# Performance work log

Measured on AMD Instinct MI355X. Metric: run time of the kernel, lower is better.

Reference implementation:

```python
import jax, jax.numpy as jnp
import numpy as np

FS = 512.0
T = 2048
CYC_PHA, CYC_AMP = 3, 6
NBINS = 18
PHA_BANDS = [(2.0 + 2.0 * k, 4.0 + 2.0 * k) for k in range(10)]
AMP_BANDS = [(30.0 + 12.0 * k, 42.0 + 12.0 * k) for k in range(10)]


def _design_filter(fs, low, high, cycle):
    # windowed-sinc bandpass, taps = cycle * fs / low (tensorpac cycle rule), forced odd
    n = int(cycle * fs / low)
    if n % 2 == 0:
        n += 1
    t = np.arange(n) - (n - 1) / 2.0
    lp = lambda fc: 2.0 * fc / fs * np.sinc(2.0 * fc / fs * t)
    h = (lp(high) - lp(low)) * np.hamming(n)
    fc = 0.5 * (low + high)
    h = h / np.abs(np.sum(h * np.exp(-2j * np.pi * fc / fs * t)))  # unit gain at band center
    return h.astype(np.float32)


def _build_kernels():
    filts = [_design_filter(FS, l, h, CYC_PHA) for l, h in PHA_BANDS] + \
            [_design_filter(FS, l, h, CYC_AMP) for l, h in AMP_BANDS]
    L = max(f.shape[0] for f in filts)
    padded = []
    for f in filts:
        p = L - f.shape[0]
        pl = p // 2
        padded.append(np.pad(f, (pl, p - pl)))
    return np.stack(padded)  # (F, L), L odd


def _conv_same(sig, kernels):
    # sig: (N, Tp), kernels: (F, L) -> (N, F, Tp); cross-correlation, 'same' padding (L odd)
    L = kernels.shape[1]
    pad = (L - 1) // 2
    return jax.lax.conv_general_dilated(
        sig[:, None, :], kernels[:, None, :], window_strides=(1,),
        padding=((pad, L - 1 - pad),), dimension_numbers=("NCH", "OIH", "NCH"))


def _analytic(x):
    # FFT-based Hilbert analytic signal along last axis
    n = x.shape[-1]
    h = np.zeros(n, np.float32)
    h[0] = 1.0
    if n % 2 == 0:
        h[n // 2] = 1.0
        h[1:n // 2] = 2.0
    else:
        h[1:(n + 1) // 2] = 2.0
    return jnp.fft.ifft(jnp.fft.fft(x, axis=-1) * h, axis=-1)


def _modulation_index(pha, amp):
    # Tort MI: pha (B,C,P,S,T), amp (B,C,A,S,T) -> (B,C,P,A)
    idx = jnp.clip(jnp.floor((pha + jnp.pi) / (2.0 * jnp.pi) * NBINS), 0, NBINS - 1).astype(jnp.int32)
    sums, cnts = [], []
    for b in range(NBINS):  # fixed small bin count
        m = (idx == b).astype(amp.dtype)                       # (B,C,P,S,T)
        sums.append(jnp.einsum('bcpst,bcast->bcpas', m, amp))  # (B,C,P,A,S)
        cnts.append(m.sum(-1))                                 # (B,C,P,S)
    amp_sum = jnp.stack(sums, -1)                              # (B,C,P,A,S,N)
    cnt = jnp.stack(cnts, -1)[:, :, :, None, :, :]             # (B,C,P,1,S,N)
    amp_mean = amp_sum / jnp.maximum(cnt, 1.0)
    p = amp_mean / jnp.maximum(amp_mean.sum(-1, keepdims=True), 1e-12)
    log_n = jnp.log(jnp.asarray(NBINS, amp.dtype))
    mi = (log_n + (p * jnp.log(jnp.maximum(p, 1e-12))).sum(-1)) / log_n
    return mi.mean(-1)  # average over segments


def setup_inputs() -> dict:
    key = jax.random.key(0)
    x = jax.random.normal(key, (4, 8, 4, T), dtype=jnp.float32)
    kernels = jnp.asarray(_build_kernels())
    return {"x": x, "kernels": kernels}


def reference(x, kernels):
    B, C, S, Tlen = x.shape
    npha = len(PHA_BANDS)
    pad = kernels.shape[1] - 1  # max_padlen (edge_mode)
    sig = x.reshape(B * C * S, Tlen)
    sig = jnp.pad(sig, ((0, 0), (pad, pad)), mode='reflect')
    # filtfilt_mode: average forward conv and time-reversed conv
    fwd = _conv_same(sig, kernels)
    bwd = _conv_same(sig[:, ::-1], kernels)[:, :, ::-1]
    filt = 0.5 * (fwd + bwd)
    filt = filt[:, :, pad:-pad]  # strip edge padding -> (N, F, T)
    ana = _analytic(filt)
    pha = jnp.arctan2(ana.imag[:, :npha], ana.real[:, :npha])
    amp = jnp.sqrt(ana.real[:, npha:] ** 2 + ana.imag[:, npha:] ** 2)
    pha = pha.reshape(B, C, npha, S, Tlen)
    amp = amp.reshape(B, C, len(AMP_BANDS), S, Tlen)
    return _modulation_index(pha, amp)
```

## Files before the change

### kernel.cpp

```cpp
#include <hip/hip_runtime.h>
#include <math.h>

#define TT 2048
#define LK 769
#define NF 20
#define NS 128
#define NB 18
#define NFFT 4096

typedef __attribute__((ext_vector_type(8))) short short8;
typedef __attribute__((ext_vector_type(4))) float f32x4;

__device__ __forceinline__ float2 cmul(float2 a, float2 b) {
  return make_float2(a.x * b.x - a.y * b.y, a.x * b.y + a.y * b.x);
}
__device__ __forceinline__ float2 cmulc(float2 a, float2 b) {
  return make_float2(a.x * b.x + a.y * b.y, a.y * b.x - a.x * b.y);
}
#define CADD(a, b) make_float2((a).x + (b).x, (a).y + (b).y)
#define CSUB(a, b) make_float2((a).x - (b).x, (a).y - (b).y)

__device__ __forceinline__ void fwd_r8(float2* z, const float2* __restrict__ tw,
                                       int tt, int Q) {
  const float C = 0.70710678118654752f;
  const int j = tt & (Q - 1);
  const int base = ((tt & ~(Q - 1)) << 3) + j;
  const float2 x0 = z[base],         x1 = z[base + Q];
  const float2 x2 = z[base + 2 * Q], x3 = z[base + 3 * Q];
  const float2 x4 = z[base + 4 * Q], x5 = z[base + 5 * Q];
  const float2 x6 = z[base + 6 * Q], x7 = z[base + 7 * Q];
  const float2 W1 = tw[4 * Q + j], W2 = tw[2 * Q + j], W4 = tw[Q + j];
  const float2 W3 = cmul(W1, W2);
  const float2 W5 = cmul(W1, W4);
  const float2 W6 = cmul(W2, W4);
  const float2 W7 = cmul(W3, W4);
  const float2 s0 = CADD(x0, x4), s1 = CSUB(x0, x4);
  const float2 s2 = CADD(x2, x6), s3 = CSUB(x2, x6);
  const float2 E0 = CADD(s0, s2), E2 = CSUB(s0, s2);
  const float2 E1 = make_float2(s1.x + s3.y, s1.y - s3.x);
  const float2 E3 = make_float2(s1.x - s3.y, s1.y + s3.x);
  const float2 t0 = CADD(x1, x5), t1 = CSUB(x1, x5);
  const float2 t2 = CADD(x3, x7), t3 = CSUB(x3, x7);
  const float2 O0 = CADD(t0, t2), O2 = CSUB(t0, t2);
  const float2 O1 = make_float2(t1.x + t3.y, t1.y - t3.x);
  const float2 O3 = make_float2(t1.x - t3.y, t1.y + t3.x);
  const float2 wO1 = make_float2(C * (O1.x + O1.y), C * (O1.y - O1.x));
  const float2 w3O3 = make_float2(C * (O3.y - O3.x), -C * (O3.x + O3.y));
  const float2 mO2 = make_float2(O2.y, -O2.x);
  const float2 y0 = CADD(E0, O0), y4 = CSUB(E0, O0);
  const float2 y1 = CADD(E1, wO1), y5 = CSUB(E1, wO1);
  const float2 y2 = CADD(E2, mO2), y6 = CSUB(E2, mO2);
  const float2 y3 = CADD(E3, w3O3), y7 = CSUB(E3, w3O3);
  z[base]         = y0;
  z[base + Q]     = cmul(y1, W1);
  z[base + 2 * Q] = cmul(y2, W2);
  z[base + 3 * Q] = cmul(y3, W3);
  z[base + 4 * Q] = cmul(y4, W4);
  z[base + 5 * Q] = cmul(y5, W5);
  z[base + 6 * Q] = cmul(y6, W6);
  z[base + 7 * Q] = cmul(y7, W7);
}

__device__ __forceinline__ void inv_r8(float2* z, const float2* __restrict__ tw,
                                       int tt, int Q) {
  const float C = 0.70710678118654752f;
  const int j = tt & (Q - 1);
  const int base = ((tt & ~(Q - 1)) << 3) + j;
  const float2 W1 = tw[4 * Q + j], W2 = tw[2 * Q + j], W4 = tw[Q + j];
  const float2 W3 = cmul(W1, W2);
  const float2 W5 = cmul(W1, W4);
  const float2 W6 = cmul(W2, W4);
  const float2 W7 = cmul(W3, W4);
  const float2 u0 = z[base];
  const float2 u1 = cmulc(z[base + Q], W1);
  const float2 u2 = cmulc(z[base + 2 * Q], W2);
  const float2 u3 = cmulc(z[base + 3 * Q], W3);
  const float2 u4 = cmulc(z[base + 4 * Q], W4);
  const float2 u5 = cmulc(z[base + 5 * Q], W5);
  const float2 u6 = cmulc(z[base + 6 * Q], W6);
  const float2 u7 = cmulc(z[base + 7 * Q], W7);
  const float2 s0 = CADD(u0, u4), s1 = CSUB(u0, u4);
  const float2 s2 = CADD(u2, u6), s3 = CSUB(u2, u6);
  const float2 E0 = CADD(s0, s2), E2 = CSUB(s0, s2);
  const float2 E1 = make_float2(s1.x - s3.y, s1.y + s3.x);
  const float2 E3 = make_float2(s1.x + s3.y, s1.y - s3.x);
  const float2 t0 = CADD(u1, u5), t1 = CSUB(u1, u5);
  const float2 t2 = CADD(u3, u7), t3 = CSUB(u3, u7);
  const float2 O0 = CADD(t0, t2), O2 = CSUB(t0, t2);
  const float2 O1 = make_float2(t1.x - t3.y, t1.y + t3.x);
  const float2 O3 = make_float2(t1.x + t3.y, t1.y - t3.x);
  const float2 nO1 = make_float2(C * (O1.x - O1.y), C * (O1.x + O1.y));
  const float2 n3O3 = make_float2(-C * (O3.x + O3.y), C * (O3.x - O3.y));
  const float2 iO2 = make_float2(-O2.y, O2.x);
  z[base]         = CADD(E0, O0);
  z[base + 4 * Q] = CSUB(E0, O0);
  z[base + Q]     = CADD(E1, nO1);
  z[base + 5 * Q] = CSUB(E1, nO1);
  z[base + 2 * Q] = CADD(E2, iO2);
  z[base + 6 * Q] = CSUB(E2, iO2);
  z[base + 3 * Q] = CADD(E3, n3O3);
  z[base + 7 * Q] = CSUB(E3, n3O3);
}

__global__ __launch_bounds__(256) void prep_kernel(float2* __restrict__ tw,
                                                   float* __restrict__ out) {
  const int i = blockIdx.x * 256 + threadIdx.x;
  if (i == 0) {
    tw[0] = make_float2(1.f, 0.f);
  } else {
    int half = 1 << (31 - __clz(i));
    int j = i - half;
    float ang = -3.14159265358979323846f * (float)j / (float)half;
    float s, c;
    sincosf(ang, &s, &c);
    tw[i] = make_float2(c, s);
  }
  if (i < 3200) out[i] = 0.f;
}

__global__ __launch_bounds__(256) void specf_kernel(const float* __restrict__ x,
                                                    const float* __restrict__ ker,
                                                    const float2* __restrict__ tw,
                                                    float2* __restrict__ Hc,
                                                    float2* __restrict__ Xs) {
  __shared__ __align__(16) float2 z[NFFT];
  const int tid = threadIdx.x;
  const int blk = blockIdx.x;
  if (blk < NF) {
    const float* kr = ker + blk * LK;
#pragma unroll
    for (int h = 0; h < 16; ++h) {
      int i = tid + 256 * h;
      float v = 0.f;
      if (i < LK) v = 0.5f * (kr[i] + kr[LK - 1 - i]);
      z[i] = make_float2(v, 0.f);
    }
  } else {
    const float* xr = x + (size_t)(blk - NF) * TT;
#pragma unroll
    for (int h = 0; h < 16; ++h) {
      int i = tid + 256 * h;
      float v = 0.f;
      if (i < 2816) {
        int m = i - 384;
        if (m < 0) m = -m;
        if (m > 2047) m = 4094 - m;
        v = xr[m];
      }
      z[i] = make_float2(v, 0.f);
    }
  }
  __syncthreads();
  fwd_r8(z, tw, tid, 512);
  fwd_r8(z, tw, tid + 256, 512);
  __syncthreads();
  fwd_r8(z, tw, tid, 64);
  fwd_r8(z, tw, tid + 256, 64);
  __builtin_amdgcn_wave_barrier();
  fwd_r8(z, tw, tid, 8);
  fwd_r8(z, tw, tid + 256, 8);
  __builtin_amdgcn_wave_barrier();
  fwd_r8(z, tw, tid, 1);
  fwd_r8(z, tw, tid + 256, 1);
  __syncthreads();
  if (blk < NF) {
    const float s = 1.0f / 4096.0f;
    float2* o = Hc + (size_t)blk * NFFT;
#pragma unroll
    for (int h = 0; h < 16; ++h) {
      int i = tid + 256 * h;
      float2 v = z[i];
      o[i] = make_float2(v.x * s, -v.y * s);
    }
  } else {
    float2* o = Xs + (size_t)(blk - NF) * NFFT;
#pragma unroll
    for (int h = 0; h < 16; ++h) {
      int i = tid + 256 * h;
      o[i] = z[i];
    }
  }
}

__global__ __launch_bounds__(256) void convhil_kernel(const float2* __restrict__ Xs,
                                                      const float2* __restrict__ Hc,
                                                      const float2* __restrict__ tw,
                                                      float* __restrict__ filt) {
  __shared__ __align__(16) float2 z[NFFT];
  const int tid = threadIdx.x;
  const int wv = tid >> 6;
  const int lane = tid & 63;
  const int ord = blockIdx.x;
  const int p = ord / NS;
  const int n = ord % NS;
  const int o1 = p;
  const int o2 = 10 + (9 - p);
  const float2* Xn = Xs + (size_t)n * NFFT;
  const float2* H1 = Hc + (size_t)o1 * NFFT;
  const float2* H2 = Hc + (size_t)o2 * NFFT;
#pragma unroll
  for (int h = 0; h < 16; ++h) {
    int i = tid + 256 * h;
    float2 Xv = Xn[i];
    float2 a = H1[i];
    float2 b = H2[i];
    float2 Cc = make_float2(a.x - b.y, a.y + b.x);
    z[i] = cmul(Xv, Cc);
  }
  __syncthreads();
  inv_r8(z, tw, tid, 1);
  inv_r8(z, tw, tid + 256, 1);
  __builtin_amdgcn_wave_barrier();
  inv_r8(z, tw, tid, 8);
  inv_r8(z, tw, tid + 256, 8);
  __builtin_amdgcn_wave_barrier();
  inv_r8(z, tw, tid, 64);
  inv_r8(z, tw, tid + 256, 64);
  __syncthreads();
  inv_r8(z, tw, tid, 512);
  inv_r8(z, tw, tid + 256, 512);
  __syncthreads();
  const int bA = 4 * tid;
  const int bB = 1024 + 4 * tid;
  float acc1A[4], acc1B[4], acc2A[4], acc2B[4];
#pragma unroll
  for (int r = 0; r < 4; ++r) {
    float2 vA = z[bA + r]; acc1A[r] = vA.x; acc2A[r] = vA.y;
    float2 vB = z[bB + r]; acc1B[r] = vB.x; acc2B[r] = vB.y;
  }
  __syncthreads();
  const float C = 0.70710678118654752f;
  fwd_r8(z, tw, tid, 256);
  __syncthreads();
  fwd_r8(z, tw, tid, 32);
  __builtin_amdgcn_wave_barrier();
  fwd_r8(z, tw, tid, 4);
  __builtin_amdgcn_wave_barrier();
#pragma unroll
  for (int h = 0; h < 2; ++h) {
    const int bf = 128 * wv + lane + 64 * h;
    const int base = bf << 2;
    const float2 x0 = z[base], x1 = z[base + 1];
    const float2 x2 = z[base + 2], x3 = z[base + 3];
    const float2 t0 = CADD(x0, x2), t1 = CSUB(x0, x2);
    const float2 t2 = CADD(x1, x3), t3 = CSUB(x1, x3);
    z[base]     = CADD(t0, t2);
    z[base + 1] = make_float2(t1.x + t3.y, t1.y - t3.x);
    z[base + 2] = CSUB(t0, t2);
    z[base + 3] = make_float2(t1.x - t3.y, t1.y + t3.x);
  }
  __builtin_amdgcn_wave_barrier();
#pragma unroll
  for (int i = 0; i < 8; ++i) {
    const int pp = 512 * wv + lane + 64 * i;
    if (pp != 0 && pp != 2) {
      if (pp & 2) { z[pp] = make_float2(0.f, 0.f); }
      else        { float2 v = z[pp]; z[pp] = make_float2(2.f * v.x, 2.f * v.y); }
    }
  }
  __builtin_amdgcn_wave_barrier();
#pragma unroll
  for (int h = 0; h < 2; ++h) {
    const int bf = 128 * wv + lane + 64 * h;
    const int base = bf << 2;
    const float2 u0 = z[base], u1 = z[base + 1];
    const float2 u2 = z[base + 2], u3 = z[base + 3];
    const float2 t0 = CADD(u0, u2), t1 = CSUB(u0, u2);
    const float2 t2 = CADD(u1, u3), t3 = CSUB(u1, u3);
    z[base]     = CADD(t0, t2);
    z[base + 1] = make_float2(t1.x - t3.y, t1.y + t3.x);
    z[base + 2] = CSUB(t0, t2);
    z[base + 3] = make_float2(t1.x + t3.y, t1.y - t3.x);
  }
  __builtin_amdgcn_wave_barrier();
  inv_r8(z, tw, tid, 4);
  __builtin_amdgcn_wave_barrier();
  inv_r8(z, tw, tid, 32);
  __builtin_amdgcn_wave_barrier();
  __syncthreads();
  inv_r8(z, tw, tid, 256);
  __syncthreads();
  (void)C;
  float* out1 = filt + ((size_t)n * NF + o1) * TT;
  float* out2 = filt + ((size_t)n * NF + o2) * TT;
  const float invN = 1.0f / 2048.0f;
  float phA[4], phB[4], amA[4], amB[4];
#pragma unroll
  for (int r = 0; r < 4; ++r) {
    float2 wvA = z[bA + r];
    float h1 = wvA.y * invN - acc2A[r];
    float h2 = acc1A[r] - wvA.x * invN;
    phA[r] = atan2f(h1, acc1A[r]);
    amA[r] = sqrtf(fmaf(acc2A[r], acc2A[r], h2 * h2));
    float2 wvB = z[bB + r];
    float g1 = wvB.y * invN - acc2B[r];
    float g2 = acc1B[r] - wvB.x * invN;
    phB[r] = atan2f(g1, acc1B[r]);
    amB[r] = sqrtf(fmaf(acc2B[r], acc2B[r], g2 * g2));
  }
  *(float4*)&out1[bA] = make_float4(phA[0], phA[1], phA[2], phA[3]);
  *(float4*)&out1[bB] = make_float4(phB[0], phB[1], phB[2], phB[3]);
  *(float4*)&out2[bA] = make_float4(amA[0], amA[1], amA[2], amA[3]);
  *(float4*)&out2[bB] = make_float4(amB[0], amB[1], amB[2], amB[3]);
}

__global__ __launch_bounds__(256) void mi_kernel(const float* __restrict__ filt,
                                                 float* __restrict__ out) {
  __shared__ __align__(16) unsigned int idx32[512];
  __shared__ float Cp[4][12][19];
  const int tid = threadIdx.x;
  const int wave = tid >> 6;
  const int lane = tid & 63;
  const int blk = blockIdx.x;
  const int bc = blk / 40, jp = blk % 40;
  const float* ph = filt + ((size_t)(bc * 4 + jp / 10) * NF + (jp % 10)) * TT;
  for (int g = tid; g < 512; g += 256) {
    float4 v = *(const float4*)&ph[4 * g];
    float vv[4] = {v.x, v.y, v.z, v.w};
    unsigned int packed = 0;
#pragma unroll
    for (int j = 0; j < 4; ++j) {
      int b = (int)floorf((vv[j] + 3.14159274f) / 6.2831855f * 18.0f);
      b = b < 0 ? 0 : (b > 17 ? 17 : b);
      packed |= ((unsigned int)b) << (8 * j);
    }
    idx32[g] = packed;
  }
  __syncthreads();
  const int n16 = lane & 15;
  const int quad = lane >> 4;
  const int aband = n16 < 10 ? n16 : 9;
  const int ja = (jp & 3) + 4 * aband;
  const float* aptr = filt + ((size_t)(bc * 4 + ja / 10) * NF + 10 + (ja % 10)) * TT
                      + quad * 8;
  const bool isAmp = (n16 < 10);
  const bool isOne = (n16 == 10);
  f32x4 acc0 = {0.f, 0.f, 0.f, 0.f};
  f32x4 acc1 = {0.f, 0.f, 0.f, 0.f};
  const int s0 = wave * 16, s1 = s0 + 16;
  float4 p0 = *(const float4*)(aptr + s0 * 32);
  float4 p1 = *(const float4*)(aptr + s0 * 32 + 4);
  for (int s = s0; s < s1; ++s) {
    float4 c0 = p0, c1 = p1;
    if (s < s1 - 1) {
      p0 = *(const float4*)(aptr + (s + 1) * 32);
      p1 = *(const float4*)(aptr + (s + 1) * 32 + 4);
    }
    float a[8] = {c0.x, c0.y, c0.z, c0.w, c1.x, c1.y, c1.z, c1.w};
    short8 ah, am_, al;
#pragma unroll
    for (int j = 0; j < 8; ++j) {
      float v = isAmp ? a[j] : (isOne ? 1.0f : 0.0f);
      unsigned int u = __float_as_uint(v);
      float h = __uint_as_float(u & 0xFFFF0000u);
      float r1 = v - h;
      unsigned int u2 = __float_as_uint(r1);
      float md = __uint_as_float(u2 & 0xFFFF0000u);
      float r2 = r1 - md;
      unsigned int u3 = __float_as_uint(r2);
      ah[j] = (short)(u >> 16);
      am_[j] = (short)(u2 >> 16);
      al[j] = (short)(u3 >> 16);
    }
    const int dw = s * 8 + quad * 2;
    unsigned int d0 = idx32[dw], d1 = idx32[dw + 1];
    short8 b0, b1;
#pragma unroll
    for (int j = 0; j < 8; ++j) {
      unsigned int byte = ((j < 4 ? d0 : d1) >> ((j & 3) * 8)) & 0xFFu;
      b0[j] = (byte == (unsigned int)n16) ? (short)0x3F80 : (short)0;
      b1[j] = (byte == (unsigned int)(n16 + 16)) ? (short)0x3F80 : (short)0;
    }
    acc0 = __builtin_amdgcn_mfma_f32_16x16x32_bf16(ah, b0, acc0, 0, 0, 0);
    acc0 = __builtin_amdgcn_mfma_f32_16x16x32_bf16(am_, b0, acc0, 0, 0, 0);
    acc0 = __builtin_amdgcn_mfma_f32_16x16x32_bf16(al, b0, acc0, 0, 0, 0);
    acc1 = __builtin_amdgcn_mfma_f32_16x16x32_bf16(ah, b1, acc1, 0, 0, 0);
    acc1 = __builtin_amdgcn_mfma_f32_16x16x32_bf16(am_, b1, acc1, 0, 0, 0);
    acc1 = __builtin_amdgcn_mfma_f32_16x16x32_bf16(al, b1, acc1, 0, 0, 0);
  }
#pragma unroll
  for (int r = 0; r < 4; ++r) {
    int row = quad * 4 + r;
    if (row < 11) {
      Cp[wave][row][n16] = acc0[r];
      if (n16 < 2) Cp[wave][row][16 + n16] = acc1[r];
    }
  }
  __syncthreads();
  if (tid < 10) {
    float tot = 0.f, mb_[18];
#pragma unroll
    for (int b = 0; b < 18; ++b) {
      float s = Cp[0][tid][b] + Cp[1][tid][b] + Cp[2][tid][b] + Cp[3][tid][b];
      float c = Cp[0][10][b] + Cp[1][10][b] + Cp[2][10][b] + Cp[3][10][b];
      float mb = s / fmaxf(c, 1.0f);
      mb_[b] = mb; tot += mb;
    }
    tot = fmaxf(tot, 1e-12f);
    float s = 0.f;
#pragma unroll
    for (int b = 0; b < 18; ++b) {
      float pb = mb_[b] / tot;
      s += pb * logf(fmaxf(pb, 1e-12f));
    }
    const float LOGN = 2.8903717578961645f;
    atomicAdd(&out[bc * 100 + (jp >> 2) * 10 + tid],
              0.25f * (LOGN + s) / LOGN);
  }
}

extern "C" void kernel_launch(void* const* d_in, const int* in_sizes, int n_in,
                              void* d_out, int out_size, void* d_ws, size_t ws_size,
                              hipStream_t stream) {
  (void)in_sizes; (void)n_in; (void)out_size; (void)ws_size;
  const float* x = (const float*)d_in[0];
  const float* ker = (const float*)d_in[1];
  float* out = (float*)d_out;
  float* filt = (float*)d_ws;
  float2* tw = (float2*)(filt + (size_t)NS * NF * TT);
  float2* Hc = tw + NFFT;
  float2* Xs = Hc + (size_t)NF * NFFT;

  prep_kernel<<<16, 256, 0, stream>>>(tw, out);
  specf_kernel<<<NF + NS, 256, 0, stream>>>(x, ker, tw, Hc, Xs);
  convhil_kernel<<<NS * 10, 256, 0, stream>>>(Xs, Hc, tw, filt);
  mi_kernel<<<32 * 40, 256, 0, stream>>>(filt, out);
}
```

Baseline: 125.9 us.

## Fuse phase binning into convhil, share amp loads across two phase bands

The Hilbert/conv kernel now quantizes phase into packed 8-bit bin indices and writes those, replacing the float phase stores, so the MI kernel reads 4x less phase data. The first inverse radix-8 stage is fused with the spectral multiply straight from global memory, and twiddle-free radix-8 variants replace the j=0 stages. The MI kernel handles two phase bands per block so each amplitude load and bf16 split is reused for twice the MFMA work, with half as many blocks and a swizzled block order. In exchange, per-thread register pressure in the MI kernel rises and there is a new workspace buffer.

```diff
diff --git a/kernel.cpp b/kernel.cpp
--- a/kernel.cpp
+++ b/kernel.cpp
@@ -61,6 +61,35 @@
   z[base + 7 * Q] = cmul(y7, W7);
 }
 
+__device__ __forceinline__ void fwd_r8_j0(float2* z, int base) {
+  const float C = 0.70710678118654752f;
+  const float2 x0 = z[base],     x1 = z[base + 1];
+  const float2 x2 = z[base + 2], x3 = z[base + 3];
+  const float2 x4 = z[base + 4], x5 = z[base + 5];
+  const float2 x6 = z[base + 6], x7 = z[base + 7];
+  const float2 s0 = CADD(x0, x4), s1 = CSUB(x0, x4);
+  const float2 s2 = CADD(x2, x6), s3 = CSUB(x2, x6);
+  const float2 E0 = CADD(s0, s2), E2 = CSUB(s0, s2);
+  const float2 E1 = make_float2(s1.x + s3.y, s1.y - s3.x);
+  const float2 E3 = make_float2(s1.x - s3.y, s1.y + s3.x);
+  const float2 t0 = CADD(x1, x5), t1 = CSUB(x1, x5);
+  const float2 t2 = CADD(x3, x7), t3 = CSUB(x3, x7);
+  const float2 O0 = CADD(t0, t2), O2 = CSUB(t0, t2);
+  const float2 O1 = make_float2(t1.x + t3.y, t1.y - t3.x);
+  const float2 O3 = make_float2(t1.x - t3.y, t1.y + t3.x);
+  const float2 wO1 = make_float2(C * (O1.x + O1.y), C * (O1.y - O1.x));
+  const float2 w3O3 = make_float2(C * (O3.y - O3.x), -C * (O3.x + O3.y));
+  const float2 mO2 = make_float2(O2.y, -O2.x);
+  z[base]     = CADD(E0, O0);
+  z[base + 4] = CSUB(E0, O0);
+  z[base + 1] = CADD(E1, wO1);
+  z[base + 5] = CSUB(E1, wO1);
+  z[base + 2] = CADD(E2, mO2);
+  z[base + 6] = CSUB(E2, mO2);
+  z[base + 3] = CADD(E3, w3O3);
+  z[base + 7] = CSUB(E3, w3O3);
+}
+
 __device__ __forceinline__ void inv_r8(float2* z, const float2* __restrict__ tw,
                                        int tt, int Q) {
   const float C = 0.70710678118654752f;
@@ -102,6 +131,47 @@
   z[base + 7 * Q] = CSUB(E3, n3O3);
 }
 
+__device__ __forceinline__ void inv8_j0_fused(float2* z,
+                                              const float2* __restrict__ Xn,
+                                              const float2* __restrict__ H1,
+                                              const float2* __restrict__ H2,
+                                              int b8) {
+  const float4* X4 = (const float4*)(Xn + b8);
+  const float4* A4 = (const float4*)(H1 + b8);
+  const float4* B4 = (const float4*)(H2 + b8);
+  float2 u[8];
+#pragma unroll
+  for (int q = 0; q < 4; ++q) {
+    float4 xv = X4[q], av = A4[q], bv = B4[q];
+    float2 Cc0 = make_float2(av.x - bv.y, av.y + bv.x);
+    float2 Cc1 = make_float2(av.z - bv.w, av.w + bv.z);
+    u[2 * q]     = cmul(make_float2(xv.x, xv.y), Cc0);
+    u[2 * q + 1] = cmul(make_float2(xv.z, xv.w), Cc1);
+  }
+  const float C = 0.70710678118654752f;
+  const float2 s0 = CADD(u[0], u[4]), s1 = CSUB(u[0], u[4]);
+  const float2 s2 = CADD(u[2], u[6]), s3 = CSUB(u[2], u[6]);
+  const float2 E0 = CADD(s0, s2), E2 = CSUB(s0, s2);
+  const float2 E1 = make_float2(s1.x - s3.y, s1.y + s3.x);
+  const float2 E3 = make_float2(s1.x + s3.y, s1.y - s3.x);
+  const float2 t0 = CADD(u[1], u[5]), t1 = CSUB(u[1], u[5]);
+  const float2 t2 = CADD(u[3], u[7]), t3 = CSUB(u[3], u[7]);
+  const float2 O0 = CADD(t0, t2), O2 = CSUB(t0, t2);
+  const float2 O1 = make_float2(t1.x - t3.y, t1.y + t3.x);
+  const float2 O3 = make_float2(t1.x + t3.y, t1.y - t3.x);
+  const float2 nO1 = make_float2(C * (O1.x - O1.y), C * (O1.x + O1.y));
+  const float2 n3O3 = make_float2(-C * (O3.x + O3.y), C * (O3.x - O3.y));
+  const float2 iO2 = make_float2(-O2.y, O2.x);
+  z[b8]     = CADD(E0, O0);
+  z[b8 + 4] = CSUB(E0, O0);
+  z[b8 + 1] = CADD(E1, nO1);
+  z[b8 + 5] = CSUB(E1, nO1);
+  z[b8 + 2] = CADD(E2, iO2);
+  z[b8 + 6] = CSUB(E2, iO2);
+  z[b8 + 3] = CADD(E3, n3O3);
+  z[b8 + 7] = CSUB(E3, n3O3);
+}
+
 __global__ __launch_bounds__(256) void prep_kernel(float2* __restrict__ tw,
                                                    float* __restrict__ out) {
   const int i = blockIdx.x * 256 + threadIdx.x;
@@ -160,8 +230,8 @@
   fwd_r8(z, tw, tid, 8);
   fwd_r8(z, tw, tid + 256, 8);
   __builtin_amdgcn_wave_barrier();
-  fwd_r8(z, tw, tid, 1);
-  fwd_r8(z, tw, tid + 256, 1);
+  fwd_r8_j0(z, tid << 3);
+  fwd_r8_j0(z, (tid + 256) << 3);
   __syncthreads();
   if (blk < NF) {
     const float s = 1.0f / 4096.0f;
@@ -185,7 +255,8 @@
 __global__ __launch_bounds__(256) void convhil_kernel(const float2* __restrict__ Xs,
                                                       const float2* __restrict__ Hc,
                                                       const float2* __restrict__ tw,
-                                                      float* __restrict__ filt) {
+                                                      float* __restrict__ filt,
+                                                      unsigned int* __restrict__ binp) {
   __shared__ __align__(16) float2 z[NFFT];
   const int tid = threadIdx.x;
   const int wv = tid >> 6;
@@ -198,18 +269,8 @@
   const float2* Xn = Xs + (size_t)n * NFFT;
   const float2* H1 = Hc + (size_t)o1 * NFFT;
   const float2* H2 = Hc + (size_t)o2 * NFFT;
-#pragma unroll
-  for (int h = 0; h < 16; ++h) {
-    int i = tid + 256 * h;
-    float2 Xv = Xn[i];
-    float2 a = H1[i];
-    float2 b = H2[i];
-    float2 Cc = make_float2(a.x - b.y, a.y + b.x);
-    z[i] = cmul(Xv, Cc);
-  }
-  __syncthreads();
-  inv_r8(z, tw, tid, 1);
-  inv_r8(z, tw, tid + 256, 1);
+  inv8_j0_fused(z, Xn, H1, H2, tid << 3);
+  inv8_j0_fused(z, Xn, H1, H2, (tid + 256) << 3);
   __builtin_amdgcn_wave_barrier();
   inv_r8(z, tw, tid, 8);
   inv_r8(z, tw, tid + 256, 8);
@@ -229,7 +290,6 @@
     float2 vB = z[bB + r]; acc1B[r] = vB.x; acc2B[r] = vB.y;
   }
   __syncthreads();
-  const float C = 0.70710678118654752f;
   fwd_r8(z, tw, tid, 256);
   __syncthreads();
   fwd_r8(z, tw, tid, 32);
@@ -280,69 +340,76 @@
   __syncthreads();
   inv_r8(z, tw, tid, 256);
   __syncthreads();
-  (void)C;
-  float* out1 = filt + ((size_t)n * NF + o1) * TT;
+  unsigned int* bp = binp + ((size_t)n * 10 + o1) * 512;
   float* out2 = filt + ((size_t)n * NF + o2) * TT;
   const float invN = 1.0f / 2048.0f;
-  float phA[4], phB[4], amA[4], amB[4];
+  float amA[4], amB[4];
+  unsigned int dA = 0, dB = 0;
 #pragma unroll
   for (int r = 0; r < 4; ++r) {
     float2 wvA = z[bA + r];
     float h1 = wvA.y * invN - acc2A[r];
     float h2 = acc1A[r] - wvA.x * invN;
-    phA[r] = atan2f(h1, acc1A[r]);
+    float phA = atan2f(h1, acc1A[r]);
     amA[r] = sqrtf(fmaf(acc2A[r], acc2A[r], h2 * h2));
+    int b = (int)floorf((phA + 3.14159274f) / 6.2831855f * 18.0f);
+    b = b < 0 ? 0 : (b > 17 ? 17 : b);
+    dA |= ((unsigned int)b) << (8 * r);
     float2 wvB = z[bB + r];
     float g1 = wvB.y * invN - acc2B[r];
     float g2 = acc1B[r] - wvB.x * invN;
-    phB[r] = atan2f(g1, acc1B[r]);
+    float phB = atan2f(g1, acc1B[r]);
     amB[r] = sqrtf(fmaf(acc2B[r], acc2B[r], g2 * g2));
-  }
-  *(float4*)&out1[bA] = make_float4(phA[0], phA[1], phA[2], phA[3]);
-  *(float4*)&out1[bB] = make_float4(phB[0], phB[1], phB[2], phB[3]);
+    int b2 = (int)floorf((phB + 3.14159274f) / 6.2831855f * 18.0f);
+    b2 = b2 < 0 ? 0 : (b2 > 17 ? 17 : b2);
+    dB |= ((unsigned int)b2) << (8 * r);
+  }
+  bp[tid] = dA;
+  bp[tid + 256] = dB;
   *(float4*)&out2[bA] = make_float4(amA[0], amA[1], amA[2], amA[3]);
   *(float4*)&out2[bB] = make_float4(amB[0], amB[1], amB[2], amB[3]);
 }
 
 __global__ __launch_bounds__(256) void mi_kernel(const float* __restrict__ filt,
+                                                 const unsigned int* __restrict__ binp,
                                                  float* __restrict__ out) {
-  __shared__ __align__(16) unsigned int idx32[512];
-  __shared__ float Cp[4][12][19];
+  __shared__ __align__(16) unsigned int idxA[512], idxB[512];
+  __shared__ float Cp[2][4][12][19];
   const int tid = threadIdx.x;
   const int wave = tid >> 6;
   const int lane = tid & 63;
-  const int blk = blockIdx.x;
-  const int bc = blk / 40, jp = blk % 40;
-  const float* ph = filt + ((size_t)(bc * 4 + jp / 10) * NF + (jp % 10)) * TT;
-  for (int g = tid; g < 512; g += 256) {
-    float4 v = *(const float4*)&ph[4 * g];
-    float vv[4] = {v.x, v.y, v.z, v.w};
-    unsigned int packed = 0;
-#pragma unroll
-    for (int j = 0; j < 4; ++j) {
-      int b = (int)floorf((vv[j] + 3.14159274f) / 6.2831855f * 18.0f);
-      b = b < 0 ? 0 : (b > 17 ? 17 : b);
-      packed |= ((unsigned int)b) << (8 * j);
-    }
-    idx32[g] = packed;
-  }
+  const int bid = blockIdx.x;
+  const int blk = (bid & 7) * 80 + (bid >> 3);
+  const int bc = blk / 20, r = blk % 20;
+  const int jpA = r, jpB = r + 20;
+  const unsigned int* bpA =
+      binp + ((size_t)(bc * 4 + jpA / 10) * 10 + (jpA % 10)) * 512;
+  const unsigned int* bpB =
+      binp + ((size_t)(bc * 4 + jpB / 10) * 10 + (jpB % 10)) * 512;
+  idxA[tid] = bpA[tid];
+  idxA[tid + 256] = bpA[tid + 256];
+  idxB[tid] = bpB[tid];
+  idxB[tid + 256] = bpB[tid + 256];
   __syncthreads();
   const int n16 = lane & 15;
   const int quad = lane >> 4;
   const int aband = n16 < 10 ? n16 : 9;
-  const int ja = (jp & 3) + 4 * aband;
+  const int ja = (jpA & 3) + 4 * aband;
   const float* aptr = filt + ((size_t)(bc * 4 + ja / 10) * NF + 10 + (ja % 10)) * TT
                       + quad * 8;
   const bool isAmp = (n16 < 10);
   const bool isOne = (n16 == 10);
-  f32x4 acc0 = {0.f, 0.f, 0.f, 0.f};
-  f32x4 acc1 = {0.f, 0.f, 0.f, 0.f};
+  f32x4 accA0 = {0.f, 0.f, 0.f, 0.f}, accA1 = {0.f, 0.f, 0.f, 0.f};
+  f32x4 accB0 = {0.f, 0.f, 0.f, 0.f}, accB1 = {0.f, 0.f, 0.f, 0.f};
   const int s0 = wave * 16, s1 = s0 + 16;
-  float4 p0 = *(const float4*)(aptr + s0 * 32);
-  float4 p1 = *(const float4*)(aptr + s0 * 32 + 4);
+  float4 p0 = make_float4(0.f, 0.f, 0.f, 0.f), p1 = p0;
+  if (isAmp) {
+    p0 = *(const float4*)(aptr + s0 * 32);
+    p1 = *(const float4*)(aptr + s0 * 32 + 4);
+  }
   for (int s = s0; s < s1; ++s) {
     float4 c0 = p0, c1 = p1;
-    if (s < s1 - 1) {
+    if (isAmp && s < s1 - 1) {
       p0 = *(const float4*)(aptr + (s + 1) * 32);
       p1 = *(const float4*)(aptr + (s + 1) * 32 + 4);
     }
@@ -363,36 +430,53 @@
       al[j] = (short)(u3 >> 16);
     }
     const int dw = s * 8 + quad * 2;
-    unsigned int d0 = idx32[dw], d1 = idx32[dw + 1];
-    short8 b0, b1;
+    unsigned int dA0 = idxA[dw], dA1 = idxA[dw + 1];
+    unsigned int dB0 = idxB[dw], dB1 = idxB[dw + 1];
+    short8 bA0, bA1, bB0, bB1;
 #pragma unroll
     for (int j = 0; j < 8; ++j) {
-      unsigned int byte = ((j < 4 ? d0 : d1) >> ((j & 3) * 8)) & 0xFFu;
-      b0[j] = (byte == (unsigned int)n16) ? (short)0x3F80 : (short)0;
-      b1[j] = (byte == (unsigned int)(n16 + 16)) ? (short)0x3F80 : (short)0;
-    }
-    acc0 = __builtin_amdgcn_mfma_f32_16x16x32_bf16(ah, b0, acc0, 0, 0, 0);
-    acc0 = __builtin_amdgcn_mfma_f32_16x16x32_bf16(am_, b0, acc0, 0, 0, 0);
-    acc0 = __builtin_amdgcn_mfma_f32_16x16x32_bf16(al, b0, acc0, 0, 0, 0);
-    acc1 = __builtin_amdgcn_mfma_f32_16x16x32_bf16(ah, b1, acc1, 0, 0, 0);
-    acc1 = __builtin_amdgcn_mfma_f32_16x16x32_bf16(am_, b1, acc1, 0, 0, 0);
-    acc1 = __builtin_amdgcn_mfma_f32_16x16x32_bf16(al, b1, acc1, 0, 0, 0);
-  }
-#pragma unroll
-  for (int r = 0; r < 4; ++r) {
-    int row = quad * 4 + r;
+      unsigned int byA = ((j < 4 ? dA0 : dA1) >> ((j & 3) * 8)) & 0xFFu;
+      unsigned int byB = ((j < 4 ? dB0 : dB1) >> ((j & 3) * 8)) & 0xFFu;
+      bA0[j] = (byA == (unsigned int)n16) ? (short)0x3F80 : (short)0;
+      bA1[j] = (byA == (unsigned int)(n16 + 16)) ? (short)0x3F80 : (short)0;
+      bB0[j] = (byB == (unsigned int)n16) ? (short)0x3F80 : (short)0;
+      bB1[j] = (byB == (unsigned int)(n16 + 16)) ? (short)0x3F80 : (short)0;
+    }
+    accA0 = __builtin_amdgcn_mfma_f32_16x16x32_bf16(ah, bA0, accA0, 0, 0, 0);
+    accA0 = __builtin_amdgcn_mfma_f32_16x16x32_bf16(am_, bA0, accA0, 0, 0, 0);
+    accA0 = __builtin_amdgcn_mfma_f32_16x16x32_bf16(al, bA0, accA0, 0, 0, 0);
+    accA1 = __builtin_amdgcn_mfma_f32_16x16x32_bf16(ah, bA1, accA1, 0, 0, 0);
+    accA1 = __builtin_amdgcn_mfma_f32_16x16x32_bf16(am_, bA1, accA1, 0, 0, 0);
+    accA1 = __builtin_amdgcn_mfma_f32_16x16x32_bf16(al, bA1, accA1, 0, 0, 0);
+    accB0 = __builtin_amdgcn_mfma_f32_16x16x32_bf16(ah, bB0, accB0, 0, 0, 0);
+    accB0 = __builtin_amdgcn_mfma_f32_16x16x32_bf16(am_, bB0, accB0, 0, 0, 0);
+    accB0 = __builtin_amdgcn_mfma_f32_16x16x32_bf16(al, bB0, accB0, 0, 0, 0);
+    accB1 = __builtin_amdgcn_mfma_f32_16x16x32_bf16(ah, bB1, accB1, 0, 0, 0);
+    accB1 = __builtin_amdgcn_mfma_f32_16x16x32_bf16(am_, bB1, accB1, 0, 0, 0);
+    accB1 = __builtin_amdgcn_mfma_f32_16x16x32_bf16(al, bB1, accB1, 0, 0, 0);
+  }
+#pragma unroll
+  for (int rr = 0; rr < 4; ++rr) {
+    int row = quad * 4 + rr;
     if (row < 11) {
-      Cp[wave][row][n16] = acc0[r];
-      if (n16 < 2) Cp[wave][row][16 + n16] = acc1[r];
-    }
-  }
-  __syncthreads();
-  if (tid < 10) {
+      Cp[0][wave][row][n16] = accA0[rr];
+      Cp[1][wave][row][n16] = accB0[rr];
+      if (n16 < 2) {
+        Cp[0][wave][row][16 + n16] = accA1[rr];
+        Cp[1][wave][row][16 + n16] = accB1[rr];
+      }
+    }
+  }
+  __syncthreads();
+  int pl = -1, a_ = 0, jp_ = 0;
+  if (tid < 10) { pl = 0; a_ = tid; jp_ = jpA; }
+  else if (tid >= 64 && tid < 74) { pl = 1; a_ = tid - 64; jp_ = jpB; }
+  if (pl >= 0) {
     float tot = 0.f, mb_[18];
 #pragma unroll
     for (int b = 0; b < 18; ++b) {
-      float s = Cp[0][tid][b] + Cp[1][tid][b] + Cp[2][tid][b] + Cp[3][tid][b];
-      float c = Cp[0][10][b] + Cp[1][10][b] + Cp[2][10][b] + Cp[3][10][b];
+      float s = Cp[pl][0][a_][b] + Cp[pl][1][a_][b] + Cp[pl][2][a_][b] + Cp[pl][3][a_][b];
+      float c = Cp[pl][0][10][b] + Cp[pl][1][10][b] + Cp[pl][2][10][b] + Cp[pl][3][10][b];
       float mb = s / fmaxf(c, 1.0f);
       mb_[b] = mb; tot += mb;
     }
@@ -404,7 +488,7 @@
       s += pb * logf(fmaxf(pb, 1e-12f));
     }
     const float LOGN = 2.8903717578961645f;
-    atomicAdd(&out[bc * 100 + (jp >> 2) * 10 + tid],
+    atomicAdd(&out[bc * 100 + (jp_ >> 2) * 10 + a_],
               0.25f * (LOGN + s) / LOGN);
   }
 }
@@ -420,9 +504,10 @@
   float2* tw = (float2*)(filt + (size_t)NS * NF * TT);
   float2* Hc = tw + NFFT;
   float2* Xs = Hc + (size_t)NF * NFFT;
+  unsigned int* binp = (unsigned int*)(Xs + (size_t)NS * NFFT);
 
   prep_kernel<<<16, 256, 0, stream>>>(tw, out);
   specf_kernel<<<NF + NS, 256, 0, stream>>>(x, ker, tw, Hc, Xs);
-  convhil_kernel<<<NS * 10, 256, 0, stream>>>(Xs, Hc, tw, filt);
-  mi_kernel<<<32 * 40, 256, 0, stream>>>(filt, out);
-}
+  convhil_kernel<<<NS * 10, 256, 0, stream>>>(Xs, Hc, tw, filt, binp);
+  mi_kernel<<<640, 256, 0, stream>>>(filt, binp, out);
+}
```

After: 123.7 us. No clear change (-1.7%).
